# Kernel tuning notes

Measured on AMD Instinct MI355X. Metric: run time of the kernel, lower is better.

## Reference

```python
import jax, jax.numpy as jnp
import numpy as np

K = 8            # top-k neighbors per channel
BN_EPS = 1e-3    # keras BatchNormalization default


def top_k_features(h, adj, k):
    # h: [N, F], adj: [N, N] (dense). Per node and per channel, take the k
    # largest masked neighbor feature values, then prepend the node's own feature.
    masked = adj[:, None, :] * h.T[None, :, :]        # [N, F, N]
    topk = jax.lax.top_k(masked, k)[0]                # [N, F, K]
    topk = jnp.transpose(topk, (0, 2, 1))             # [N, K, F]
    return jnp.concatenate([h[:, None, :], topk], axis=1)  # [N, K+1, F]


def conv1d(x, w):
    # x: [N, L, Cin], w: [kw, Cin, Cout], VALID 1D conv
    return jax.lax.conv_general_dilated(x, w, (1,), 'VALID',
                                        dimension_numbers=('NWC', 'WIO', 'NWC'))


def batchnorm(x, gamma, beta, mean, var):
    return gamma * (x - mean) * jax.lax.rsqrt(var + BN_EPS) + beta


def setup_inputs():
    key = jax.random.key(0)
    ks = jax.random.split(key, 16)
    N, Fin, H, Cout, NF = 1600, 1433, 32, 7, 8
    x = jax.random.normal(ks[0], (N, Fin), jnp.float32)
    # sparse binary adjacency, avg degree ~16
    adj = (jax.random.uniform(ks[1], (N, N)) < 0.01).astype(jnp.float32)
    mask = jax.random.uniform(ks[2], (N,)) < 0.5

    def g(k, shape, fan_in):
        return jax.random.normal(k, shape, jnp.float32) * (1.0 / np.sqrt(fan_in))

    W0 = g(ks[3], (Fin, H), Fin)                 # DenseConvolution (GCN) weight
    # LGConv block 1: F=32 -> mid (32+8)//2=20 -> 8; kernels 5,5 reduce 9->5->1
    W1a = g(ks[4], (5, 32, 20), 5 * 32)
    W1b = g(ks[5], (5, 20, NF), 5 * 20)
    # LGConv block 2: F=40 -> mid (40+8)//2=24 -> 8
    W2a = g(ks[6], (5, 40, 24), 5 * 40)
    W2b = g(ks[7], (5, 24, NF), 5 * 24)
    Wout = g(ks[8], (H + 2 * NF, Cout), H + 2 * NF)  # 48 -> 7
    bn = {}
    for i, kk in ((1, 9), (2, 12)):
        bn[f'g{i}'] = 1.0 + 0.1 * jax.random.normal(ks[kk], (NF,), jnp.float32)
        bn[f'b{i}'] = 0.1 * jax.random.normal(ks[kk + 1], (NF,), jnp.float32)
        bn[f'm{i}'] = 0.1 * jax.random.normal(ks[kk + 2], (NF,), jnp.float32)
        bn[f'v{i}'] = jax.random.uniform(ks[kk], (NF,), jnp.float32, 0.5, 1.5)
    return {'x': x, 'adj': adj, 'W0': W0, 'W1a': W1a, 'W1b': W1b,
            'W2a': W2a, 'W2b': W2b, 'Wout': Wout,
            'g1': bn['g1'], 'b1': bn['b1'], 'm1': bn['m1'], 'v1': bn['v1'],
            'g2': bn['g2'], 'b2': bn['b2'], 'm2': bn['m2'], 'v2': bn['v2'],
            'mask': mask}


def reference(x, adj, W0, W1a, W1b, W2a, W2b, Wout,
              g1, b1, m1, v1, g2, b2, m2, v2, mask):
    # inference mode: dropout = identity
    h = adj @ (x @ W0)                                # GCN layer, hidden=32
    for Wa, Wb, g, b, m, v in ((W1a, W1b, g1, b1, m1, v1),
                               (W2a, W2b, g2, b2, m2, v2)):
        t = top_k_features(h, adj, K)                 # [N, K+1, F]
        c = conv1d(t, Wa)                             # [N, 5, mid]
        c = conv1d(c, Wb)[:, 0, :]                    # [N, 8]
        c = batchnorm(c, g, b, m, v)
        h = jnp.concatenate([h, c], axis=-1)          # 32 -> 40 -> 48
    logits = adj @ (h @ Wout)                         # [N, 7]
    # Mask layer (boolean_mask); static-shape variant: zero out masked rows
    return jnp.where(mask[:, None], logits, 0.0)
```

## Files before the change

kernel.cpp:

```cpp
#include <hip/hip_runtime.h>


constexpr int NN   = 1600;
constexpr int FIN  = 1433;
constexpr int HGCN = 32;
constexpr int NBS  = 96;
constexpr float BN_EPS = 1e-3f;

constexpr int KS    = 16;
constexpr int CHUNK = 90;
constexpr int BM    = 32;
constexpr int SXS   = 92;
constexpr int RB    = NN / BM;
constexpr int CSRB  = 400;
constexpr int K1B   = CSRB + 1 + RB * KS;
constexpr int GB    = 256;
constexpr int NT    = 512;

__device__ __forceinline__ void astore(float* p, float v) {
    __hip_atomic_store(p, v, __ATOMIC_RELAXED, __HIP_MEMORY_SCOPE_AGENT);
}
__device__ __forceinline__ void astorei(int* p, int v) {
    __hip_atomic_store(p, v, __ATOMIC_RELAXED, __HIP_MEMORY_SCOPE_AGENT);
}
__device__ __forceinline__ int aloadi(const int* p) {
    return __hip_atomic_load(p, __ATOMIC_RELAXED, __HIP_MEMORY_SCOPE_AGENT);
}

__device__ __forceinline__ void gbar(int* cntrel, int phase) {
    int* cnt = cntrel + phase * GB;
    int* rel = cntrel + 896 + phase;
    __syncthreads();
    if (blockIdx.x == 0) {
        int s = threadIdx.x;
        if (s >= 1 && s < GB) {
            while (aloadi(&cnt[s]) == 0) __builtin_amdgcn_s_sleep(1);
        }
        __syncthreads();
        if (threadIdx.x == 0) astorei(rel, 1);
    } else {
        if (threadIdx.x == 0) {
            astorei(&cnt[blockIdx.x], 1);
            while (aloadi(rel) == 0) __builtin_amdgcn_s_sleep(1);
        }
    }
    __syncthreads();
}

__global__ __launch_bounds__(256) void k1(const float* __restrict__ x,
                                          const float* __restrict__ W0,
                                          const float* __restrict__ adj,
                                          const float* __restrict__ W1a,
                                          const float* __restrict__ W2a,
                                          int* __restrict__ deg,
                                          unsigned short* __restrict__ nbr,
                                          const unsigned char* __restrict__ mb,
                                          int* __restrict__ flag,
                                          float* __restrict__ wsT1,
                                          float* __restrict__ wsT2,
                                          float* __restrict__ h0) {
    __shared__ float sx[BM][SXS];
    __shared__ float sw[CHUNK * HGCN];
    int b = blockIdx.x, t = threadIdx.x;

    if (b < CSRB) {
        int lane = t & 63;
        int row  = b * 4 + (t >> 6);
        const float*  ar  = adj + (size_t)row * NN;
        const float4* ar4 = (const float4*)ar;
        unsigned short* nb = nbr + (size_t)row * NBS;
        int cnt = 0;
        #pragma unroll
        for (int it = 0; it < 6; ++it) {
            float4 v = ar4[it * 64 + lane];
            int base = it * 256 + 4 * lane;
            #pragma unroll
            for (int c = 0; c < 4; ++c) {
                float vc = (c == 0) ? v.x : (c == 1) ? v.y : (c == 2) ? v.z : v.w;
                bool p = (vc != 0.0f);
                unsigned long long m = __ballot(p);
                if (p) {
                    int off = cnt + __popcll(m & ((1ull << lane) - 1ull));
                    if (off < NBS) nb[off] = (unsigned short)(base + c);
                }
                cnt += __popcll(m);
            }
        }
        {
            float v = ar[1536 + lane];
            bool p = (v != 0.0f);
            unsigned long long m = __ballot(p);
            if (p) {
                int off = cnt + __popcll(m & ((1ull << lane) - 1ull));
                if (off < NBS) nb[off] = (unsigned short)(1536 + lane);
            }
            cnt += __popcll(m);
        }
        if (lane == 0) deg[row] = cnt < NBS ? cnt : NBS;
        return;
    }

    if (b == CSRB) {
        if (t < 64) {
            int lane = t;
            bool odd = false, flt = false;
            for (int i = lane; i < NN; i += 64) {
                unsigned char v = mb[i];
                if (v) {
                    int r = i & 3;
                    if (r != 0) odd = true;
                    if (r >= 2 && (v == 0x3F || v == 0x80)) flt = true;
                }
            }
            unsigned long long mo = __ballot(odd);
            unsigned long long mf = __ballot(flt);
            if (lane == 0) *flag = mf ? 2 : (mo ? 1 : 0);
        }
        for (int s = t; s < 5 * 32 * 20; s += 256) {
            int kw = s / 640, r = s - kw * 640, ci = r / 20, o = r - ci * 20;
            wsT1[(kw * 20 + o) * 36 + ci] = W1a[s];
        }
        for (int s = t; s < 5 * 40 * 24; s += 256) {
            int kw = s / 960, r = s - kw * 960, ci = r / 24, o = r - ci * 24;
            wsT2[(kw * 24 + o) * 44 + ci] = W2a[s];
        }
        return;
    }

    int tile = b - (CSRB + 1);
    int rb   = tile % RB;
    int ks   = tile / RB;
    int lane = t & 31;
    int row0 = rb * BM;
    int k0   = ks * CHUNK;
    int vk   = FIN - k0; if (vk > CHUNK) vk = CHUNK;

    {
        int g = t >> 5;
        #pragma unroll
        for (int j = 0; j < 4; ++j) {
            int r = g + 8 * j;
            const float* xr = x + (size_t)(row0 + r) * FIN + k0;
            #pragma unroll
            for (int m = 0; m < 3; ++m) {
                int k = lane + 32 * m;
                if (k < CHUNK) sx[r][k] = (k < vk) ? xr[k] : 0.0f;
            }
        }
    }
    {
        const float4* w4  = (const float4*)(W0 + (size_t)k0 * HGCN);
        float4*       sw4 = (float4*)sw;
        int vf4 = vk * 8;
        for (int i = t; i < CHUNK * 8; i += 256)
            sw4[i] = (i < vf4) ? w4[i] : make_float4(0.f, 0.f, 0.f, 0.f);
    }
    __syncthreads();

    int col = lane;
    int rq  = t >> 5;
    float acc0 = 0.f, acc1 = 0.f, acc2 = 0.f, acc3 = 0.f;
    #pragma unroll 4
    for (int kk = 0; kk < 88; kk += 4) {
        float4 a0 = *(const float4*)&sx[rq     ][kk];
        float4 a1 = *(const float4*)&sx[rq +  8][kk];
        float4 a2 = *(const float4*)&sx[rq + 16][kk];
        float4 a3 = *(const float4*)&sx[rq + 24][kk];
        float w0v = sw[(kk + 0) * HGCN + col];
        float w1v = sw[(kk + 1) * HGCN + col];
        float w2v = sw[(kk + 2) * HGCN + col];
        float w3v = sw[(kk + 3) * HGCN + col];
        acc0 += a0.x * w0v + a0.y * w1v + a0.z * w2v + a0.w * w3v;
        acc1 += a1.x * w0v + a1.y * w1v + a1.z * w2v + a1.w * w3v;
        acc2 += a2.x * w0v + a2.y * w1v + a2.z * w2v + a2.w * w3v;
        acc3 += a3.x * w0v + a3.y * w1v + a3.z * w2v + a3.w * w3v;
    }
    #pragma unroll
    for (int kk = 88; kk < CHUNK; ++kk) {
        float wv = sw[kk * HGCN + col];
        acc0 += sx[rq     ][kk] * wv;
        acc1 += sx[rq +  8][kk] * wv;
        acc2 += sx[rq + 16][kk] * wv;
        acc3 += sx[rq + 24][kk] * wv;
    }

    atomicAdd(&h0[(row0 + rq     ) * HGCN + col], acc0);
    atomicAdd(&h0[(row0 + rq +  8) * HGCN + col], acc1);
    atomicAdd(&h0[(row0 + rq + 16) * HGCN + col], acc2);
    atomicAdd(&h0[(row0 + rq + 24) * HGCN + col], acc3);
}

template<int F, int MID, int FP, bool WRITEZ>
__device__ __forceinline__ void lgconv_phase(int b, int wave, int lane,
        const int* __restrict__ deg, const unsigned short* __restrict__ nbr,
        const float* sWt, const float* __restrict__ Wb,
        const float* __restrict__ g, const float* __restrict__ bb,
        const float* __restrict__ mm, const float* __restrict__ vv,
        const float* __restrict__ h32, const float* __restrict__ c1in,
        const float* __restrict__ Wout,
        float* __restrict__ outbuf, float* T, float* C1, float* sz) {
    int row = b + 256 * wave;
    if (row >= NN) return;
    int d = deg[row];
    const unsigned short* nb = nbr + (size_t)row * NBS;

    if (lane < F) {
        float t0=0.f,t1=0.f,t2=0.f,t3=0.f,t4=0.f,t5=0.f,t6=0.f,t7=0.f;
        #define BUBBLE(val_) { float val=val_, c;                       \
            c = t0; t0 = fmaxf(c, val); val = fminf(c, val);            \
            c = t1; t1 = fmaxf(c, val); val = fminf(c, val);            \
            c = t2; t2 = fmaxf(c, val); val = fminf(c, val);            \
            c = t3; t3 = fmaxf(c, val); val = fminf(c, val);            \
            c = t4; t4 = fmaxf(c, val); val = fminf(c, val);            \
            c = t5; t5 = fmaxf(c, val); val = fminf(c, val);            \
            c = t6; t6 = fmaxf(c, val); val = fminf(c, val);            \
            c = t7; t7 = fmaxf(c, val); val = fminf(c, val); }
        #define LDV(n_) ((F == 32) ? h32[(n_) * HGCN + lane]            \
            : ((lane < 32) ? h32[(n_) * HGCN + lane] : c1in[(n_) * 8 + (lane - 32)]))
        int it = 0;
        for (; it + 8 <= d; it += 8) {
            float v[8];
            #pragma unroll
            for (int j = 0; j < 8; ++j) v[j] = LDV((int)nb[it + j]);
            #pragma unroll
            for (int j = 0; j < 8; ++j) BUBBLE(v[j]);
        }
        for (; it < d; ++it) BUBBLE(LDV((int)nb[it]));
        T[0*F+lane] = LDV(row);
        T[1*F+lane] = t0; T[2*F+lane] = t1; T[3*F+lane] = t2; T[4*F+lane] = t3;
        T[5*F+lane] = t4; T[6*F+lane] = t5; T[7*F+lane] = t6; T[8*F+lane] = t7;
        #undef LDV
        #undef BUBBLE
    }
    for (int oi = lane; oi < 5 * MID; oi += 64) {
        int p = oi / MID, o = oi - p * MID;
        float ax = 0.f, ay = 0.f, az = 0.f, aw = 0.f;
        #pragma unroll
        for (int kw = 0; kw < 5; ++kw) {
            const float4* t4 = (const float4*)&T[(p + kw) * F];
            const float4* w4 = (const float4*)&sWt[(kw * MID + o) * FP];
            #pragma unroll
            for (int q = 0; q < F / 4; ++q) {
                float4 tv = t4[q], wv = w4[q];
                ax += tv.x * wv.x; ay += tv.y * wv.y;
                az += tv.z * wv.z; aw += tv.w * wv.w;
            }
        }
        C1[p * MID + o] = (ax + ay) + (az + aw);
    }
    if (lane < 8) {
        float acc = 0.f;
        #pragma unroll
        for (int kw = 0; kw < 5; ++kw)
            for (int ci = 0; ci < MID; ++ci)
                acc += C1[kw * MID + ci] * Wb[(kw * MID + ci) * 8 + lane];
        float y = g[lane] * (acc - mm[lane]) * rsqrtf(vv[lane] + BN_EPS) + bb[lane];
        if (WRITEZ) sz[lane] = y;
        else        astore(&outbuf[row * 8 + lane], y);
    }
    if (WRITEZ) {
        if (lane < 8) {
            float z = 0.f;
            if (lane < 7) {
                #pragma unroll
                for (int k = 0; k < 40; ++k) z += T[k] * Wout[k * 7 + lane];
                #pragma unroll
                for (int j = 0; j < 8; ++j)  z += sz[j] * Wout[(40 + j) * 7 + lane];
            }
            astore(&outbuf[row * 8 + lane], z);
        }
    }
}

__global__ __launch_bounds__(NT) void k2(
        const int* __restrict__ deg, const unsigned short* __restrict__ nbr,
        const float* __restrict__ h0,
        float* __restrict__ h32, float* __restrict__ c1, float* __restrict__ zbuf,
        const float* __restrict__ wsT1, const float* __restrict__ wsT2,
        const float* __restrict__ W1b,
        const float* __restrict__ g1, const float* __restrict__ b1,
        const float* __restrict__ m1, const float* __restrict__ v1,
        const float* __restrict__ W2b,
        const float* __restrict__ g2, const float* __restrict__ b2,
        const float* __restrict__ m2, const float* __restrict__ v2,
        const float* __restrict__ Wout, const void* __restrict__ mask,
        const int* __restrict__ flag, int* __restrict__ cntrel,
        float* __restrict__ out) {
    __shared__ float sWt1[3600];
    __shared__ float sWt2[5280];
    __shared__ float T   [8][360];
    __shared__ float C1s [8][120];
    __shared__ float szs [8][8];
    int t = threadIdx.x, b = blockIdx.x;
    int wave = t >> 6, lane = t & 63;

    {
        const float4* s1 = (const float4*)wsT1;
        const float4* s2 = (const float4*)wsT2;
        float4* d1 = (float4*)sWt1;
        float4* d2 = (float4*)sWt2;
        for (int i = t; i < 900;  i += NT) d1[i] = s1[i];
        for (int i = t; i < 1320; i += NT) d2[i] = s2[i];
    }

    {
        int row = b + 256 * (t >> 5);
        if (row < NN) {
            int f = t & 31;
            int d = deg[row];
            const unsigned short* nb = nbr + (size_t)row * NBS;
            float acc = 0.f;
            int it = 0;
            for (; it + 8 <= d; it += 8) {
                float v[8];
                #pragma unroll
                for (int j = 0; j < 8; ++j) v[j] = h0[(int)nb[it + j] * HGCN + f];
                #pragma unroll
                for (int j = 0; j < 8; ++j) acc += v[j];
            }
            for (; it < d; ++it) acc += h0[(int)nb[it] * HGCN + f];
            astore(&h32[row * HGCN + f], acc);
        }
    }
    gbar(cntrel, 0);

    lgconv_phase<32, 20, 36, false>(b, wave, lane, deg, nbr, sWt1, W1b,
                                    g1, b1, m1, v1, h32, nullptr, Wout, c1,
                                    T[wave], C1s[wave], szs[wave]);
    gbar(cntrel, 1);

    lgconv_phase<40, 24, 44, true>(b, wave, lane, deg, nbr, sWt2, W2b,
                                   g2, b2, m2, v2, h32, c1, Wout, zbuf,
                                   T[wave], C1s[wave], szs[wave]);
    gbar(cntrel, 2);

    {
        int row = b + 256 * wave;
        if (row < NN) {
            int d = deg[row];
            const unsigned short* nb = nbr + (size_t)row * NBS;
            int ng = lane >> 3, c = lane & 7;
            float acc = 0.f;
            for (int it = ng; it < d; it += 8)
                acc += zbuf[(int)nb[it] * 8 + c];
            acc += __shfl_xor(acc, 8);
            acc += __shfl_xor(acc, 16);
            acc += __shfl_xor(acc, 32);
            if (lane < 7) {
                int fl = *flag;
                bool mk;
                if (fl == 2)      mk = ((const float*)mask)[row] != 0.0f;
                else if (fl == 1) mk = ((const unsigned char*)mask)[row] != 0;
                else              mk = ((const int*)mask)[row] != 0;
                out[row * 7 + lane] = mk ? acc : 0.0f;
            }
        }
    }
}

extern "C" void kernel_launch(void* const* d_in, const int* in_sizes, int n_in,
                              void* d_out, int out_size, void* d_ws, size_t ws_size,
                              hipStream_t stream) {
    const float* x    = (const float*)d_in[0];
    const float* adj  = (const float*)d_in[1];
    const float* W0   = (const float*)d_in[2];
    const float* W1a  = (const float*)d_in[3];
    const float* W1b  = (const float*)d_in[4];
    const float* W2a  = (const float*)d_in[5];
    const float* W2b  = (const float*)d_in[6];
    const float* Wout = (const float*)d_in[7];
    const float* g1 = (const float*)d_in[8];
    const float* b1 = (const float*)d_in[9];
    const float* m1 = (const float*)d_in[10];
    const float* v1 = (const float*)d_in[11];
    const float* g2 = (const float*)d_in[12];
    const float* b2 = (const float*)d_in[13];
    const float* m2 = (const float*)d_in[14];
    const float* v2 = (const float*)d_in[15];
    const void*  mask = d_in[16];

    char* ws = (char*)d_ws;
    int*            cntrel = (int*)(ws + 0);
    float*          h0     = (float*)(ws + 20480);
    int*            flag   = (int*)(ws + 225280);
    int*            deg    = (int*)(ws + 225792);
    unsigned short* nbr    = (unsigned short*)(ws + 232192);
    float*          h32    = (float*)(ws + 539392);
    float*          c1     = (float*)(ws + 744192);
    float*          zbuf   = (float*)(ws + 795392);
    float*          wsT1   = (float*)(ws + 846592);
    float*          wsT2   = (float*)(ws + 860992);

    float* out = (float*)d_out;

    hipMemsetAsync(ws, 0, 225280, stream);
    k1<<<K1B, 256, 0, stream>>>(x, W0, adj, W1a, W2a, deg, nbr,
                                (const unsigned char*)mask, flag, wsT1, wsT2, h0);
    k2<<<GB, NT, 0, stream>>>(deg, nbr, h0, h32, c1, zbuf, wsT1, wsT2,
                              W1b, g1, b1, m1, v1,
                              W2b, g2, b2, m2, v2,
                              Wout, mask, flag, cntrel, out);
}
```

Baseline: 52.70 us.

## Interleave conv weights by float4 channel groups and split neighbor sum across half-waves

The first-conv weights are repacked into a [kw][ci/4][o] float4 layout, so adjacent lanes (consecutive outputs o) read consecutive float4s from shared memory instead of padded strided rows. The top-k feature tile gets a fixed stride TS. The smaller weight buffers shrink shared memory and move the wsT2 offset. The first GCN aggregation now uses all 64 lanes of a wave, each half summing alternate neighbors, combined with a shuffle, which halves per-lane gather latency but changes the rows handled per block.

```diff
diff --git a/kernel.cpp b/kernel.cpp
--- a/kernel.cpp
+++ b/kernel.cpp
@@ -116,13 +116,19 @@
             unsigned long long mf = __ballot(flt);
             if (lane == 0) *flag = mf ? 2 : (mo ? 1 : 0);
         }
-        for (int s = t; s < 5 * 32 * 20; s += 256) {
-            int kw = s / 640, r = s - kw * 640, ci = r / 20, o = r - ci * 20;
-            wsT1[(kw * 20 + o) * 36 + ci] = W1a[s];
-        }
-        for (int s = t; s < 5 * 40 * 24; s += 256) {
-            int kw = s / 960, r = s - kw * 960, ci = r / 24, o = r - ci * 24;
-            wsT2[(kw * 24 + o) * 44 + ci] = W2a[s];
+        for (int f = t; f < 800; f += 256) {
+            int kw = f / 160, r = f - kw * 160, q = r / 20, o = r - q * 20;
+            const float* wsrc = W1a + kw * 640 + 4 * q * 20 + o;
+            float4 v;
+            v.x = wsrc[0]; v.y = wsrc[20]; v.z = wsrc[40]; v.w = wsrc[60];
+            ((float4*)wsT1)[f] = v;
+        }
+        for (int f = t; f < 1200; f += 256) {
+            int kw = f / 240, r = f - kw * 240, q = r / 24, o = r - q * 24;
+            const float* wsrc = W2a + kw * 960 + 4 * q * 24 + o;
+            float4 v;
+            v.x = wsrc[0]; v.y = wsrc[24]; v.z = wsrc[48]; v.w = wsrc[72];
+            ((float4*)wsT2)[f] = v;
         }
         return;
     }
@@ -190,7 +196,7 @@
     atomicAdd(&h0[(row0 + rq + 24) * HGCN + col], acc3);
 }
 
-template<int F, int MID, int FP, bool WRITEZ>
+template<int F, int MID, int TS, bool WRITEZ>
 __device__ __forceinline__ void lgconv_phase(int b, int wave, int lane,
         const int* __restrict__ deg, const unsigned short* __restrict__ nbr,
         const float* sWt, const float* __restrict__ Wb,
@@ -226,9 +232,9 @@
             for (int j = 0; j < 8; ++j) BUBBLE(v[j]);
         }
         for (; it < d; ++it) BUBBLE(LDV((int)nb[it]));
-        T[0*F+lane] = LDV(row);
-        T[1*F+lane] = t0; T[2*F+lane] = t1; T[3*F+lane] = t2; T[4*F+lane] = t3;
-        T[5*F+lane] = t4; T[6*F+lane] = t5; T[7*F+lane] = t6; T[8*F+lane] = t7;
+        T[0*TS+lane] = LDV(row);
+        T[1*TS+lane] = t0; T[2*TS+lane] = t1; T[3*TS+lane] = t2; T[4*TS+lane] = t3;
+        T[5*TS+lane] = t4; T[6*TS+lane] = t5; T[7*TS+lane] = t6; T[8*TS+lane] = t7;
         #undef LDV
         #undef BUBBLE
     }
@@ -237,11 +243,11 @@
         float ax = 0.f, ay = 0.f, az = 0.f, aw = 0.f;
         #pragma unroll
         for (int kw = 0; kw < 5; ++kw) {
-            const float4* t4 = (const float4*)&T[(p + kw) * F];
-            const float4* w4 = (const float4*)&sWt[(kw * MID + o) * FP];
+            const float4* t4 = (const float4*)&T[(p + kw) * TS];
+            const float4* w4 = ((const float4*)sWt) + kw * (F / 4) * MID + o;
             #pragma unroll
             for (int q = 0; q < F / 4; ++q) {
-                float4 tv = t4[q], wv = w4[q];
+                float4 tv = t4[q], wv = w4[q * MID];
                 ax += tv.x * wv.x; ay += tv.y * wv.y;
                 az += tv.z * wv.z; aw += tv.w * wv.w;
             }
@@ -286,9 +292,9 @@
         const float* __restrict__ Wout, const void* __restrict__ mask,
         const int* __restrict__ flag, int* __restrict__ cntrel,
         float* __restrict__ out) {
-    __shared__ float sWt1[3600];
-    __shared__ float sWt2[5280];
-    __shared__ float T   [8][360];
+    __shared__ float sWt1[3200];
+    __shared__ float sWt2[4800];
+    __shared__ float T   [8][400];
     __shared__ float C1s [8][120];
     __shared__ float szs [8][8];
     int t = threadIdx.x, b = blockIdx.x;
@@ -299,27 +305,28 @@
         const float4* s2 = (const float4*)wsT2;
         float4* d1 = (float4*)sWt1;
         float4* d2 = (float4*)sWt2;
-        for (int i = t; i < 900;  i += NT) d1[i] = s1[i];
-        for (int i = t; i < 1320; i += NT) d2[i] = s2[i];
+        for (int i = t; i < 800;  i += NT) d1[i] = s1[i];
+        for (int i = t; i < 1200; i += NT) d2[i] = s2[i];
     }
 
     {
-        int row = b + 256 * (t >> 5);
+        int row = b + 256 * wave;
         if (row < NN) {
-            int f = t & 31;
+            int f = lane & 31, half = lane >> 5;
             int d = deg[row];
             const unsigned short* nb = nbr + (size_t)row * NBS;
             float acc = 0.f;
-            int it = 0;
-            for (; it + 8 <= d; it += 8) {
+            int it = half;
+            for (; it + 16 <= d; it += 16) {
                 float v[8];
                 #pragma unroll
-                for (int j = 0; j < 8; ++j) v[j] = h0[(int)nb[it + j] * HGCN + f];
+                for (int j = 0; j < 8; ++j) v[j] = h0[(int)nb[it + 2 * j] * HGCN + f];
                 #pragma unroll
                 for (int j = 0; j < 8; ++j) acc += v[j];
             }
-            for (; it < d; ++it) acc += h0[(int)nb[it] * HGCN + f];
-            astore(&h32[row * HGCN + f], acc);
+            for (; it < d; it += 2) acc += h0[(int)nb[it] * HGCN + f];
+            acc += __shfl_xor(acc, 32);
+            if (half == 0) astore(&h32[row * HGCN + f], acc);
         }
     }
     gbar(cntrel, 0);
@@ -389,7 +396,7 @@
     float*          c1     = (float*)(ws + 744192);
     float*          zbuf   = (float*)(ws + 795392);
     float*          wsT1   = (float*)(ws + 846592);
-    float*          wsT2   = (float*)(ws + 860992);
+    float*          wsT2   = (float*)(ws + 859392);
 
     float* out = (float*)d_out;
 
```

Result: faster. 50.21 us (-4.7%).
